# Optimization experiments

Measured on AMD Instinct MI355X. Metric: run time of the kernel, lower is better.

Reference implementation:

```python
import jax, jax.numpy as jnp
import numpy as np

B, S, H = 1, 2048, 2048
NH, NKV, HD = 16, 2, 128
ROPE_THETA = 1000000.0
BF16 = jnp.bfloat16


def setup_inputs() -> dict:
    key = jax.random.key(0)
    ks = jax.random.split(key, 6)
    hidden_states = jax.random.normal(ks[0], (B, S, H), dtype=jnp.float32)
    # causal additive mask, 0 on/below diagonal, large negative above
    causal = jnp.tril(jnp.ones((S, S), dtype=bool))
    attention_mask = jnp.where(causal, 0.0, -1e9).astype(jnp.float32)[None, None, :, :]
    position_ids = jnp.arange(S, dtype=jnp.int32)[None, :]
    sc = 1.0 / np.sqrt(H)
    Wq = jax.random.normal(ks[1], (H, H), dtype=jnp.float32) * sc
    bq = jnp.zeros((H,), dtype=jnp.float32)
    Wk = jax.random.normal(ks[2], (H, NKV * HD), dtype=jnp.float32) * sc
    bk = jnp.zeros((NKV * HD,), dtype=jnp.float32)
    Wv = jax.random.normal(ks[3], (H, NKV * HD), dtype=jnp.float32) * sc
    bv = jnp.zeros((NKV * HD,), dtype=jnp.float32)
    Wo = jax.random.normal(ks[4], (H, H), dtype=jnp.float32) * sc
    return {"hidden_states": hidden_states, "attention_mask": attention_mask,
            "position_ids": position_ids, "Wq": Wq, "bq": bq, "Wk": Wk, "bk": bk,
            "Wv": Wv, "bv": bv, "Wo": Wo}


def _rope_tables(pos):
    # pos: [S] int. freqs: [HD//2]
    freqs = 1.0 / (ROPE_THETA ** (jnp.arange(0, HD, 2, dtype=jnp.float32) / HD))
    ang = pos.astype(jnp.float32)[:, None] * freqs[None, :]  # [S, HD//2]
    return jnp.cos(ang), jnp.sin(ang)


def _apply_rope(x, cos, sin):
    # x: [B,S,nheads,HD]; cos/sin: [S,HD//2] -> broadcast over heads
    c = cos[None, :, None, :]
    s = sin[None, :, None, :]
    x1, x2 = x[..., : HD // 2], x[..., HD // 2 :]
    return jnp.concatenate([x1 * c - x2 * s, x1 * s + x2 * c], axis=-1)


def reference(hidden_states, attention_mask, position_ids, Wq, bq, Wk, bk, Wv, bv, Wo):
    x = hidden_states.astype(BF16)
    # bf16 projections (flax Dense dtype=bfloat16)
    q = (x @ Wq.astype(BF16) + bq.astype(BF16)).reshape(B, S, NH, HD)
    k = (x @ Wk.astype(BF16) + bk.astype(BF16)).reshape(B, S, NKV, HD)
    v = (x @ Wv.astype(BF16) + bv.astype(BF16)).reshape(B, S, NKV, HD)
    cos, sin = _rope_tables(position_ids[0])
    q = _apply_rope(q.astype(jnp.float32), cos, sin).astype(jnp.float32)
    k = _apply_rope(k.astype(jnp.float32), cos, sin).astype(jnp.float32)
    cache_k, cache_v = k, v  # cache holds un-repeated kv (k post-rope, v bf16)
    rep = NH // NKV  # GQA repeat
    k = jnp.repeat(k, rep, axis=2)
    vr = jnp.repeat(v, rep, axis=2)
    # [B,NH,S,HD]
    qh = q.transpose(0, 2, 1, 3)
    kh = k.transpose(0, 2, 1, 3)
    vh = vr.transpose(0, 2, 1, 3).astype(jnp.float32)
    scale = 1.0 / jnp.sqrt(jnp.float32(HD))
    scores = jnp.einsum('bhqd,bhkd->bhqk', qh, kh) * scale + attention_mask
    probs = jnp.clip(jax.nn.softmax(scores.astype(jnp.float32), axis=-1), 1e-09, 1 - 1e-09)
    attn = jnp.einsum('bhqk,bhkd->bhqd', probs, vh)
    attn = attn.transpose(0, 2, 1, 3).reshape(B, S, H)
    out = (attn.astype(BF16) @ Wo.astype(BF16)).astype(jnp.float32)
    return out, cache_k, cache_v
```

## Files before the change

kernel.cpp:

```cpp
#include <hip/hip_runtime.h>
#include <hip/hip_bf16.h>
#include <math.h>

#define S_LEN 2048
#define HDIM  2048
#define N_H   16
#define N_KV  2
#define HD_   128
#define NQKV  2560

typedef __attribute__((ext_vector_type(8))) short bf16x8;
typedef __attribute__((ext_vector_type(4))) float f32x4;
typedef __attribute__((ext_vector_type(16))) float f32x16;

#define GLDS16(gsrc, ldst)                                                      \
  __builtin_amdgcn_global_load_lds(                                             \
      (const __attribute__((address_space(1))) void*)(gsrc),                    \
      (__attribute__((address_space(3))) void*)(ldst), 16, 0, 0)

__device__ __forceinline__ ushort f2b(float x) {
  union { __hip_bfloat16 b; ushort u; } c;
  c.b = __float2bfloat16(x);
  return c.u;
}
__device__ __forceinline__ float b2f(ushort u) {
  union { float f; unsigned v; } c;
  c.v = ((unsigned)u) << 16;
  return c.f;
}
__device__ __forceinline__ uint pk2(float a, float b) {
  return (uint)f2b(a) | ((uint)f2b(b) << 16);
}

__global__ __launch_bounds__(256) void k_prep(const float* __restrict__ hidden,
                                              const float* __restrict__ Wq,
                                              const float* __restrict__ Wk,
                                              const float* __restrict__ Wv,
                                              ushort* __restrict__ x_b,
                                              ushort* __restrict__ wt) {
  __shared__ float t[64][65];
  const int bid = blockIdx.x;
  const int tid = threadIdx.x;
  if (bid < 4096) {
    const int i = bid * 256 + tid;
    float4 v = ((const float4*)hidden)[i];
    ushort4 o;
    o.x = f2b(v.x); o.y = f2b(v.y); o.z = f2b(v.z); o.w = f2b(v.w);
    ((ushort4*)x_b)[i] = o;
    return;
  }
  int tb = bid - 4096;
  const float* src;
  ushort* dst;
  int C, bx, by;
  if (tb < 1024) {
    src = Wq; dst = wt; C = 2048; bx = tb & 31; by = tb >> 5;
  } else if (tb < 1152) {
    tb -= 1024; src = Wk; dst = wt + (size_t)2048 * 2048; C = 256; bx = tb & 3; by = tb >> 2;
  } else {
    tb -= 1152; src = Wv; dst = wt + (size_t)2304 * 2048; C = 256; bx = tb & 3; by = tb >> 2;
  }
  const int c0 = bx * 64, r0 = by * 64;
  const int tx = tid & 63, ty = tid >> 6;
#pragma unroll
  for (int i = 0; i < 16; ++i)
    t[i * 4 + ty][tx] = src[(size_t)(r0 + i * 4 + ty) * C + (c0 + tx)];
  __syncthreads();
#pragma unroll
  for (int i = 0; i < 16; ++i)
    dst[(size_t)(c0 + i * 4 + ty) * 2048 + (r0 + tx)] = f2b(t[tx][i * 4 + ty]);
}

__global__ __launch_bounds__(256) void k_transpose_bf16(const float* __restrict__ src,
                                                        ushort* __restrict__ dst,
                                                        int R, int C) {
  __shared__ float t[64][65];
  int c0 = blockIdx.x * 64, r0 = blockIdx.y * 64;
  int tx = threadIdx.x & 63, ty = threadIdx.x >> 6;
#pragma unroll
  for (int i = 0; i < 16; ++i)
    t[i * 4 + ty][tx] = src[(size_t)(r0 + i * 4 + ty) * C + (c0 + tx)];
  __syncthreads();
#pragma unroll
  for (int i = 0; i < 16; ++i)
    dst[(size_t)(c0 + i * 4 + ty) * R + (r0 + tx)] = f2b(t[tx][i * 4 + ty]);
}

__global__ __launch_bounds__(256) void k_gemm_bt(const ushort* __restrict__ A,
                                                 const ushort* __restrict__ Bt,
                                                 ushort* __restrict__ Cp,
                                                 int M, int N, int Kfull, int Khalf) {
  __shared__ ushort lA[128 * 64];
  __shared__ ushort lB[128 * 64];
  const int tid = threadIdx.x;
  const int w = tid >> 6, lane = tid & 63;
  const int lr = lane & 15, lg = lane >> 4;
  const int bm = blockIdx.x * 128, bn = blockIdx.y * 128;
  const int wm = (w >> 1) * 64, wn = (w & 1) * 64;
  const int kbeg = blockIdx.z * Khalf;
  ushort* Cout = Cp + (size_t)blockIdx.z * M * N;
  f32x4 acc[4][4] = {};

  for (int k0 = kbeg; k0 < kbeg + Khalf; k0 += 64) {
    __syncthreads();
#pragma unroll
    for (int it = 0; it < 4; ++it) {
      const int idx = it * 256 + tid;
      const int row = idx >> 3;
      const int gsl = (idx & 7) ^ (row & 7);
      GLDS16(A + (size_t)(bm + row) * Kfull + k0 + gsl * 8,
             lA + (it * 256 + w * 64) * 8);
      GLDS16(Bt + (size_t)(bn + row) * Kfull + k0 + gsl * 8,
             lB + (it * 256 + w * 64) * 8);
    }
    __syncthreads();
#pragma unroll
    for (int ks = 0; ks < 2; ++ks) {
      bf16x8 af[4], bf[4];
#pragma unroll
      for (int i = 0; i < 4; ++i) {
        const int ra = wm + i * 16 + lr;
        af[i] = *(const bf16x8*)(lA + ra * 64 + (((ks * 4 + lg) ^ (ra & 7)) * 8));
        const int rb = wn + i * 16 + lr;
        bf[i] = *(const bf16x8*)(lB + rb * 64 + (((ks * 4 + lg) ^ (rb & 7)) * 8));
      }
      __builtin_amdgcn_s_setprio(1);
#pragma unroll
      for (int mi = 0; mi < 4; ++mi)
#pragma unroll
        for (int ni = 0; ni < 4; ++ni)
          acc[mi][ni] =
              __builtin_amdgcn_mfma_f32_16x16x32_bf16(af[mi], bf[ni], acc[mi][ni], 0, 0, 0);
      __builtin_amdgcn_s_setprio(0);
    }
  }

#pragma unroll
  for (int mi = 0; mi < 4; ++mi)
#pragma unroll
    for (int ni = 0; ni < 4; ++ni)
#pragma unroll
      for (int r = 0; r < 4; ++r) {
        const int row = bm + wm + mi * 16 + lg * 4 + r;
        const int col = bn + wn + ni * 16 + lr;
        Cout[(size_t)row * N + col] = f2b(acc[mi][ni][r]);
      }
}

__global__ __launch_bounds__(256) void k_epirope(const ushort* __restrict__ p0,
                                                 const ushort* __restrict__ p1,
                                                 const float* __restrict__ bq,
                                                 const float* __restrict__ bk,
                                                 const float* __restrict__ bv,
                                                 const int* __restrict__ pos_ids,
                                                 ushort* __restrict__ q_r,
                                                 ushort* __restrict__ k_r,
                                                 ushort* __restrict__ v_t,
                                                 float* __restrict__ cache_k,
                                                 float* __restrict__ cache_v) {
  const int s = blockIdx.x;
  const int t = threadIdx.x;
  __shared__ float row[NQKV];
  const uint* a = (const uint*)(p0 + (size_t)s * NQKV);
  const uint* b = (const uint*)(p1 + (size_t)s * NQKV);
#pragma unroll
  for (int j = 0; j < 5; ++j) {
    const int c2 = t + 256 * j;
    const uint u0 = a[c2], u1 = b[c2];
    const int c = 2 * c2;
    const float v0 = b2f((ushort)u0) + b2f((ushort)(u1 & 0xffff));
    const float v1 = b2f((ushort)(u0 >> 16)) + b2f((ushort)(u1 >> 16));
    const float bias0 = (c < 2048) ? bq[c] : (c < 2304 ? bk[c - 2048] : bv[c - 2304]);
    const float bias1 = (c + 1 < 2048) ? bq[c + 1]
                                       : (c + 1 < 2304 ? bk[c + 1 - 2048] : bv[c + 1 - 2304]);
    row[c] = b2f(f2b(b2f(f2b(v0)) + b2f(f2b(bias0))));
    row[c + 1] = b2f(f2b(b2f(f2b(v1)) + b2f(f2b(bias1))));
  }
  __syncthreads();

  const int i = t & 63, g = t >> 6;
  const float SCALE = 0.08838834764831845f;
  const float pos = (float)pos_ids[s];
  const float freq = (float)(1.0 / pow(1000000.0, (double)i / 64.0));
  float sn, cs;
  sincosf(pos * freq, &sn, &cs);

#pragma unroll
  for (int j = 0; j < 4; ++j) {
    const int h = j * 4 + g;
    const float x1 = row[h * 128 + i];
    const float x2 = row[h * 128 + 64 + i];
    const float o1 = x1 * cs - x2 * sn;
    const float o2 = x1 * sn + x2 * cs;
    const size_t qo = ((size_t)h * S_LEN + s) * 128;
    q_r[qo + i] = f2b(o1 * SCALE);
    q_r[qo + 64 + i] = f2b(o2 * SCALE);
  }
  if (g < 2) {
    const int kv = g;
    const float x1 = row[2048 + kv * 128 + i];
    const float x2 = row[2048 + kv * 128 + 64 + i];
    const float o1 = x1 * cs - x2 * sn;
    const float o2 = x1 * sn + x2 * cs;
    const size_t ko = ((size_t)kv * S_LEN + s) * 128;
    k_r[ko + i] = f2b(o1);
    k_r[ko + 64 + i] = f2b(o2);
    const size_t co = ((size_t)s * 2 + kv) * 128;
    cache_k[co + i] = o1;
    cache_k[co + 64 + i] = o2;
  }
  {
    const int kv = t >> 7, d = t & 127;
    const float vval = row[2304 + kv * 128 + d];
    cache_v[((size_t)s * 2 + kv) * 128 + d] = vval;
    v_t[((size_t)kv * 128 + d) * S_LEN + s] = f2b(vval);
  }
}

__global__ __launch_bounds__(256) void k_addround(const ushort* __restrict__ p0,
                                                  const ushort* __restrict__ p1,
                                                  float* __restrict__ out, int n2) {
  int i = blockIdx.x * 256 + threadIdx.x;
  if (i >= n2) return;
  const uint a = ((const uint*)p0)[i];
  const uint b = ((const uint*)p1)[i];
  float2 o;
  o.x = b2f(f2b(b2f((ushort)(a & 0xffff)) + b2f((ushort)(b & 0xffff))));
  o.y = b2f(f2b(b2f((ushort)(a >> 16)) + b2f((ushort)(b >> 16))));
  ((float2*)out)[i] = o;
}

__global__ __launch_bounds__(256, 2) void k_attn(const ushort* __restrict__ q_r,
                                                 const ushort* __restrict__ k_r,
                                                 const ushort* __restrict__ v_t,
                                                 ushort* __restrict__ attn_b) {
  __shared__ ushort smem[2][2][8192];
  __shared__ float stats[2][32][2];

  const int bi = blockIdx.x;
  const int h = bi & 15;
  const int tq = (bi >> 4) & 15;
  const int Q = (bi >> 8) ? (31 - tq) : tq;
  const int kvh = h >> 3;

  const int tid = threadIdx.x, w = tid >> 6, lane = tid & 63;
  const int g = w >> 1, wq = w & 1, tg = tid & 127;
  const int l31 = lane & 31, hb = lane >> 5;
  const int S_steps = Q + 1;
  const int qmaxw = Q * 64 + wq * 32 + 31;

  bf16x8 qf[8];
  {
    const ushort* qp =
        q_r + ((size_t)(h * S_LEN + Q * 64 + wq * 32 + l31)) * 128 + hb * 8;
#pragma unroll
    for (int f = 0; f < 8; ++f) qf[f] = *(const bf16x8*)(qp + f * 16);
  }

  f32x16 acc[4] = {};
  float m = -INFINITY, l = 0.f;

#define STAGE(BUF, T32)                                                           \
  do {                                                                            \
    const int kb_ = (T32) * 32;                                                   \
    _Pragma("unroll") for (int i = 0; i < 4; ++i) {                               \
      const int idx = i * 128 + tg;                                               \
      {                                                                           \
        const int key = idx >> 4, sl = idx & 15;                                  \
        GLDS16(k_r + ((size_t)(kvh * S_LEN + kb_ + key)) * 128 +                  \
                   ((sl ^ (key & 7)) * 8),                                        \
               &smem[g][BUF][i * 1024 + wq * 512]);                               \
      }                                                                           \
      {                                                                           \
        const int d = idx >> 2, p = idx & 3;                                      \
        const int gs = (p - (d >> 1)) & 3;                                        \
        GLDS16(v_t + ((size_t)(kvh * HD_ + d)) * S_LEN + kb_ + gs * 8,            \
               &smem[g][BUF][4096 + i * 1024 + wq * 512]);                        \
      }                                                                           \
    }                                                                             \
  } while (0)

  STAGE(0, g);
  int buf = 0;

  for (int s = 0; s < S_steps; ++s) {
    __syncthreads();
    if (s + 1 < S_steps) STAGE(buf ^ 1, 2 * (s + 1) + g);
    const int kb = (2 * s + g) * 32;

    if (kb <= qmaxw) {
      const ushort* lK = &smem[g][buf][0];
      const ushort* lV = &smem[g][buf][4096];

      f32x16 p0 = {};
      __builtin_amdgcn_s_setprio(1);
#pragma unroll
      for (int f = 0; f < 8; ++f) {
        const int key = l31;
        const bf16x8 kf8 =
            *(const bf16x8*)(lK + key * 128 + (((2 * f + hb) ^ (key & 7)) * 8));
        p0 = __builtin_amdgcn_mfma_f32_32x32x16_bf16(kf8, qf[f], p0, 0, 0, 0);
      }
      __builtin_amdgcn_s_setprio(0);

      const int q = Q * 64 + wq * 32 + l31;
      float sv[16];
#pragma unroll
      for (int r = 0; r < 16; ++r) {
        const int key = kb + (r & 3) + 8 * (r >> 2) + 4 * hb;
        sv[r] = (key <= q) ? p0[r] : -INFINITY;
      }
      float t8[8];
#pragma unroll
      for (int j = 0; j < 8; ++j) t8[j] = fmaxf(sv[j], sv[j + 8]);
#pragma unroll
      for (int st = 4; st >= 1; st >>= 1)
#pragma unroll
        for (int j = 0; j < 4; ++j)
          if (j < st) t8[j] = fmaxf(t8[j], t8[j + st]);
      const float mxw = fmaxf(t8[0], __shfl_xor(t8[0], 32));

      if (__any(mxw > m + 8.f)) {
        const float mn = fmaxf(m, mxw);
        const float sc = __expf(m - mn);
#pragma unroll
        for (int g2 = 0; g2 < 4; ++g2)
#pragma unroll
          for (int r = 0; r < 16; ++r) acc[g2][r] *= sc;
        l *= sc;
        m = mn;
      }
#pragma unroll
      for (int r = 0; r < 16; ++r) sv[r] = __expf(sv[r] - m);
      float ts[8];
#pragma unroll
      for (int j = 0; j < 8; ++j) ts[j] = sv[j] + sv[j + 8];
#pragma unroll
      for (int st = 4; st >= 1; st >>= 1)
#pragma unroll
        for (int j = 0; j < 4; ++j)
          if (j < st) ts[j] += ts[j + st];
      l += ts[0];

      uint pk8[8];
#pragma unroll
      for (int j = 0; j < 8; ++j) pk8[j] = pk2(sv[2 * j], sv[2 * j + 1]);
      union FragU { uint wd[4]; bf16x8 v; };
      FragU frag[2];
#pragma unroll
      for (int c1 = 0; c1 < 2; ++c1) {
        uint mine0, mine1, rcv0, rcv1;
        {
          const uint pa_ = pk8[0 + 4 * c1];
          const uint pb_ = pk8[2 + 4 * c1];
          const uint mn_ = hb ? pb_ : pa_;
          const uint xc_ = hb ? pa_ : pb_;
          mine0 = mn_;
          rcv0 = (uint)__shfl_xor((int)xc_, 32);
        }
        {
          const uint pa_ = pk8[1 + 4 * c1];
          const uint pb_ = pk8[3 + 4 * c1];
          const uint mn_ = hb ? pb_ : pa_;
          const uint xc_ = hb ? pa_ : pb_;
          mine1 = mn_;
          rcv1 = (uint)__shfl_xor((int)xc_, 32);
        }
        frag[c1].wd[0] = hb ? rcv0 : mine0;
        frag[c1].wd[1] = hb ? rcv1 : mine1;
        frag[c1].wd[2] = hb ? mine0 : rcv0;
        frag[c1].wd[3] = hb ? mine1 : rcv1;
      }

      __builtin_amdgcn_s_setprio(1);
#pragma unroll
      for (int g2 = 0; g2 < 4; ++g2) {
        const int d = g2 * 32 + l31;
#pragma unroll
        for (int c = 0; c < 2; ++c) {
          const int phys = ((2 * c + hb) + (d >> 1)) & 3;
          const bf16x8 vf = *(const bf16x8*)(lV + d * 32 + phys * 8);
          acc[g2] = __builtin_amdgcn_mfma_f32_32x32x16_bf16(vf, frag[c].v, acc[g2], 0, 0, 0);
        }
      }
      __builtin_amdgcn_s_setprio(0);
    }
    buf ^= 1;
  }
  __syncthreads();

  float* mrg = (float*)&smem[0][0][0];
  float* ldsO = (float*)&smem[1][0][0];
  if (g == 1) {
    const float lt1 = l + __shfl_xor(l, 32);
#pragma unroll
    for (int g2 = 0; g2 < 4; ++g2)
#pragma unroll
      for (int r = 0; r < 16; ++r) {
        const int d5 = (r & 3) + 8 * (r >> 2) + 4 * hb;
        mrg[wq * 4096 + (g2 * 32 + d5) * 32 + l31] = acc[g2][r];
      }
    if (hb == 0) {
      stats[wq][l31][0] = m;
      stats[wq][l31][1] = lt1;
    }
  }
  __syncthreads();
  if (g == 0) {
    const float m1 = stats[wq][l31][0];
    const float l1 = stats[wq][l31][1];
    const float l0 = l + __shfl_xor(l, 32);
    const float ms = fmaxf(m, m1);
    const float f0 = __expf(m - ms);
    const float f1 = __expf(m1 - ms);
    const float inv = 1.0f / (l0 * f0 + l1 * f1);
#pragma unroll
    for (int g2 = 0; g2 < 4; ++g2)
#pragma unroll
      for (int r = 0; r < 16; ++r) {
        const int d5 = (r & 3) + 8 * (r >> 2) + 4 * hb;
        const float o1v = mrg[wq * 4096 + (g2 * 32 + d5) * 32 + l31];
        const float val = (acc[g2][r] * f0 + o1v * f1) * inv;
        ldsO[wq * 4096 + l31 * 128 + g2 * 32 + (d5 ^ l31)] = val;
      }
#pragma unroll
    for (int pass = 0; pass < 8; ++pass) {
      const int qrow = pass * 4 + (lane >> 4);
      const int d0 = (lane & 15) * 8;
      float v[8];
#pragma unroll
      for (int j = 0; j < 8; ++j)
        v[j] = ldsO[wq * 4096 + qrow * 128 + (((d0 + j) & 31) ^ qrow) + (d0 & 96)];
      uint4 o;
      o.x = pk2(v[0], v[1]); o.y = pk2(v[2], v[3]);
      o.z = pk2(v[4], v[5]); o.w = pk2(v[6], v[7]);
      const size_t qg = (size_t)(Q * 64 + wq * 32 + qrow);
      *(uint4*)(attn_b + qg * HDIM + h * 128 + d0) = o;
    }
  }
#undef STAGE
}

extern "C" void kernel_launch(void* const* d_in, const int* in_sizes, int n_in,
                              void* d_out, int out_size, void* d_ws, size_t ws_size,
                              hipStream_t stream) {
  const float* hidden = (const float*)d_in[0];
  const int* pos_ids = (const int*)d_in[2];
  const float* Wq = (const float*)d_in[3];
  const float* bq = (const float*)d_in[4];
  const float* Wk = (const float*)d_in[5];
  const float* bk = (const float*)d_in[6];
  const float* Wv = (const float*)d_in[7];
  const float* bv = (const float*)d_in[8];
  const float* Wo = (const float*)d_in[9];

  float* out = (float*)d_out;
  float* cache_k = out + (size_t)S_LEN * HDIM;
  float* cache_v = cache_k + (size_t)S_LEN * N_KV * HD_;

  char* ws = (char*)d_ws;
  ushort* x_b = (ushort*)(ws);
  ushort* wt = (ushort*)(ws + (8ull << 20));
  ushort* qkvp = (ushort*)(ws + (18ull << 20));
  ushort* q_r = (ushort*)(ws);
  ushort* k_r = (ushort*)(ws + (8ull << 20));
  ushort* v_t = (ushort*)(ws + (9ull << 20));
  ushort* wo_t = (ushort*)(ws + (10ull << 20));
  ushort* attn_b = (ushort*)(ws + (18ull << 20));
  ushort* outp = (ushort*)(ws + (26ull << 20));

  k_prep<<<dim3(5376), 256, 0, stream>>>(hidden, Wq, Wk, Wv, x_b, wt);
  k_gemm_bt<<<dim3(16, 20, 2), 256, 0, stream>>>(x_b, wt, qkvp, 2048, 2560, 2048, 1024);
  k_transpose_bf16<<<dim3(32, 32), 256, 0, stream>>>(Wo, wo_t, 2048, 2048);
  k_epirope<<<dim3(S_LEN), 256, 0, stream>>>(qkvp, qkvp + (size_t)2048 * 2560, bq, bk, bv,
                                             pos_ids, q_r, k_r, v_t, cache_k, cache_v);
  k_attn<<<dim3(512), 256, 0, stream>>>(q_r, k_r, v_t, attn_b);
  k_gemm_bt<<<dim3(16, 16, 2), 256, 0, stream>>>(attn_b, wo_t, outp, 2048, 2048, 2048, 1024);
  k_addround<<<dim3((2048 * 2048 / 2 + 255) / 256), 256, 0, stream>>>(
      outp, outp + (size_t)2048 * 2048, out, 2048 * 2048 / 2);
}
```

Before: 142.1 us.

## Double-buffer GEMM LDS tiles, split QK accumulation chains, simplify attention block order

```diff
diff --git a/kernel.cpp b/kernel.cpp
--- a/kernel.cpp
+++ b/kernel.cpp
@@ -90,50 +90,55 @@
                                                  const ushort* __restrict__ Bt,
                                                  ushort* __restrict__ Cp,
                                                  int M, int N, int Kfull, int Khalf) {
-  __shared__ ushort lA[128 * 64];
-  __shared__ ushort lB[128 * 64];
+  __shared__ ushort lA[2][128 * 32];
+  __shared__ ushort lB[2][128 * 32];
   const int tid = threadIdx.x;
   const int w = tid >> 6, lane = tid & 63;
   const int lr = lane & 15, lg = lane >> 4;
   const int bm = blockIdx.x * 128, bn = blockIdx.y * 128;
   const int wm = (w >> 1) * 64, wn = (w & 1) * 64;
   const int kbeg = blockIdx.z * Khalf;
+  const int NT = Khalf / 32;
   ushort* Cout = Cp + (size_t)blockIdx.z * M * N;
   f32x4 acc[4][4] = {};
 
-  for (int k0 = kbeg; k0 < kbeg + Khalf; k0 += 64) {
+#define GSTAGE(BUF, K0)                                                          \
+  do {                                                                           \
+    _Pragma("unroll") for (int it = 0; it < 2; ++it) {                           \
+      const int idx = it * 256 + tid;                                            \
+      const int row = idx >> 2;                                                  \
+      const int gsl = (idx & 3) ^ (row & 3);                                     \
+      GLDS16(A + (size_t)(bm + row) * Kfull + (K0) + gsl * 8,                    \
+             &lA[BUF][(it * 256 + w * 64) * 8]);                                 \
+      GLDS16(Bt + (size_t)(bn + row) * Kfull + (K0) + gsl * 8,                   \
+             &lB[BUF][(it * 256 + w * 64) * 8]);                                 \
+    }                                                                            \
+  } while (0)
+
+  GSTAGE(0, kbeg);
+  int buf = 0;
+  for (int t = 0; t < NT; ++t) {
     __syncthreads();
-#pragma unroll
-    for (int it = 0; it < 4; ++it) {
-      const int idx = it * 256 + tid;
-      const int row = idx >> 3;
-      const int gsl = (idx & 7) ^ (row & 7);
-      GLDS16(A + (size_t)(bm + row) * Kfull + k0 + gsl * 8,
-             lA + (it * 256 + w * 64) * 8);
-      GLDS16(Bt + (size_t)(bn + row) * Kfull + k0 + gsl * 8,
-             lB + (it * 256 + w * 64) * 8);
+    if (t + 1 < NT) GSTAGE(buf ^ 1, kbeg + (t + 1) * 32);
+    bf16x8 af[4], bf[4];
+#pragma unroll
+    for (int i = 0; i < 4; ++i) {
+      const int ra = wm + i * 16 + lr;
+      af[i] = *(const bf16x8*)(&lA[buf][ra * 32 + ((lg ^ (ra & 3)) * 8)]);
+      const int rb = wn + i * 16 + lr;
+      bf[i] = *(const bf16x8*)(&lB[buf][rb * 32 + ((lg ^ (rb & 3)) * 8)]);
     }
-    __syncthreads();
-#pragma unroll
-    for (int ks = 0; ks < 2; ++ks) {
-      bf16x8 af[4], bf[4];
-#pragma unroll
-      for (int i = 0; i < 4; ++i) {
-        const int ra = wm + i * 16 + lr;
-        af[i] = *(const bf16x8*)(lA + ra * 64 + (((ks * 4 + lg) ^ (ra & 7)) * 8));
-        const int rb = wn + i * 16 + lr;
-        bf[i] = *(const bf16x8*)(lB + rb * 64 + (((ks * 4 + lg) ^ (rb & 7)) * 8));
-      }
-      __builtin_amdgcn_s_setprio(1);
-#pragma unroll
-      for (int mi = 0; mi < 4; ++mi)
-#pragma unroll
-        for (int ni = 0; ni < 4; ++ni)
-          acc[mi][ni] =
-              __builtin_amdgcn_mfma_f32_16x16x32_bf16(af[mi], bf[ni], acc[mi][ni], 0, 0, 0);
-      __builtin_amdgcn_s_setprio(0);
-    }
-  }
+    __builtin_amdgcn_s_setprio(1);
+#pragma unroll
+    for (int mi = 0; mi < 4; ++mi)
+#pragma unroll
+      for (int ni = 0; ni < 4; ++ni)
+        acc[mi][ni] =
+            __builtin_amdgcn_mfma_f32_16x16x32_bf16(af[mi], bf[ni], acc[mi][ni], 0, 0, 0);
+    __builtin_amdgcn_s_setprio(0);
+    buf ^= 1;
+  }
+#undef GSTAGE
 
 #pragma unroll
   for (int mi = 0; mi < 4; ++mi)
@@ -239,8 +244,7 @@
 
   const int bi = blockIdx.x;
   const int h = bi & 15;
-  const int tq = (bi >> 4) & 15;
-  const int Q = (bi >> 8) ? (31 - tq) : tq;
+  const int Q = bi >> 4;
   const int kvh = h >> 3;
 
   const int tid = threadIdx.x, w = tid >> 6, lane = tid & 63;
@@ -292,16 +296,22 @@
       const ushort* lK = &smem[g][buf][0];
       const ushort* lV = &smem[g][buf][4096];
 
-      f32x16 p0 = {};
+      f32x16 pA = {}, pB = {};
       __builtin_amdgcn_s_setprio(1);
 #pragma unroll
-      for (int f = 0; f < 8; ++f) {
-        const int key = l31;
+      for (int f = 0; f < 4; ++f) {
         const bf16x8 kf8 =
-            *(const bf16x8*)(lK + key * 128 + (((2 * f + hb) ^ (key & 7)) * 8));
-        p0 = __builtin_amdgcn_mfma_f32_32x32x16_bf16(kf8, qf[f], p0, 0, 0, 0);
+            *(const bf16x8*)(lK + l31 * 128 + (((2 * f + hb) ^ (l31 & 7)) * 8));
+        pA = __builtin_amdgcn_mfma_f32_32x32x16_bf16(kf8, qf[f], pA, 0, 0, 0);
+      }
+#pragma unroll
+      for (int f = 4; f < 8; ++f) {
+        const bf16x8 kf8 =
+            *(const bf16x8*)(lK + l31 * 128 + (((2 * f + hb) ^ (l31 & 7)) * 8));
+        pB = __builtin_amdgcn_mfma_f32_32x32x16_bf16(kf8, qf[f], pB, 0, 0, 0);
       }
       __builtin_amdgcn_s_setprio(0);
+      const f32x16 p0 = pA + pB;
 
       const int q = Q * 64 + wq * 32 + l31;
       float sv[16];
```

Result: slower. 154.6 us (+8.8%).
